# Kernel tuning notes

Hardware: AMD Instinct MI355X
Metric: run time of the kernel (lower is better)

Reference implementation:

```python
import jax, jax.numpy as jnp
import numpy as np

B, S, D, H, DH = 4, 2048, 1024, 16, 64  # batch, seq, d_model, heads, head_dim


def setup_inputs() -> dict:
    key = jax.random.key(0)
    ks = jax.random.split(key, 5)
    sc_in = 1.0 / np.sqrt(D)
    return {
        "x": jax.random.normal(ks[0], (B, S, D), dtype=jnp.float32),
        "Wq": jax.random.normal(ks[1], (H, D, DH), dtype=jnp.float32) * sc_in,
        "Wk": jax.random.normal(ks[2], (H, D, DH), dtype=jnp.float32) * sc_in,
        "Wv": jax.random.normal(ks[3], (H, D, DH), dtype=jnp.float32) * sc_in,
        "Wo": jax.random.normal(ks[4], (D, D), dtype=jnp.float32) * sc_in,
        "bo": jnp.zeros((D,), dtype=jnp.float32),
    }


def reference(x, Wq, Wk, Wv, Wo, bo):
    # Per-head Q/K/V projections (all heads batched in one einsum each).
    q = jnp.einsum("bsd,hde->bhse", x, Wq)  # [B,H,S,DH]
    k = jnp.einsum("bsd,hde->bhse", x, Wk)
    v = jnp.einsum("bsd,hde->bhse", x, Wv)
    scale = 1.0 / jnp.sqrt(jnp.asarray(DH, dtype=x.dtype))
    scores = jnp.einsum("bhse,bhte->bhst", q, k) * scale  # [B,H,S,S]
    causal = jnp.tril(jnp.ones((S, S), dtype=bool))
    scores = jnp.where(causal, scores, jnp.asarray(-jnp.inf, dtype=scores.dtype))
    attn = jax.nn.softmax(scores, axis=-1)
    heads = jnp.einsum("bhst,bhte->bhse", attn, v)  # [B,H,S,DH]
    # Concat heads (head-major order matches torch.cat of per-head outputs).
    concat = heads.transpose(0, 2, 1, 3).reshape(B, S, D)
    out = jnp.einsum("bsd,df->bsf", concat, Wo) + bo
    return out  # dropout_rate = 0.0 -> identity
```

## Files before the change

kernel.cpp:

```cpp
#include <hip/hip_runtime.h>
#include <hip/hip_bf16.h>

typedef __attribute__((ext_vector_type(8))) short short8;
typedef __attribute__((ext_vector_type(4))) short short4x;
typedef __attribute__((ext_vector_type(4))) float floatx4;

__device__ __forceinline__ short f2bf(float f) {
    unsigned u = __float_as_uint(f);
    u = u + 0x7fffu + ((u >> 16) & 1u);
    return (short)(u >> 16);
}
__device__ __forceinline__ short f2bf_rz(float f) {
    return (short)(__float_as_uint(f) >> 16);
}

static constexpr int B_ = 4, S_ = 2048, D_ = 1024, H_ = 16, DH_ = 64;
static constexpr float QSCALE = 0.125f * 1.4426950408889634f;

__global__ __launch_bounds__(256) void convert_x(const float* __restrict__ in,
                                                 short* __restrict__ out, int n8) {
    int i = blockIdx.x * 256 + threadIdx.x;
    if (i >= n8) return;
    const float4* p = (const float4*)(in + (size_t)i * 8);
    float4 a = p[0], b = p[1];
    short8 v;
    v[0] = f2bf(a.x); v[1] = f2bf(a.y); v[2] = f2bf(a.z); v[3] = f2bf(a.w);
    v[4] = f2bf(b.x); v[5] = f2bf(b.y); v[6] = f2bf(b.z); v[7] = f2bf(b.w);
    *(short8*)(out + (size_t)i * 8) = v;
}

__global__ __launch_bounds__(256) void prep_weights(const float* __restrict__ Wq,
                                                    const float* __restrict__ Wk,
                                                    const float* __restrict__ Wv,
                                                    const float* __restrict__ Wo,
                                                    short* __restrict__ WqT,
                                                    short* __restrict__ WkT,
                                                    short* __restrict__ WvT,
                                                    short* __restrict__ WoT) {
    __shared__ alignas(16) float t[64 * 68];
    int z = blockIdx.z;
    const float* in;
    short* out;
    int N, M = D_, n0;
    if (z < 3) {
        const float* I = (z == 0) ? Wq : (z == 1) ? Wk : Wv;
        short* O = (z == 0) ? WqT : (z == 1) ? WkT : WvT;
        in = I + (size_t)blockIdx.y * D_ * DH_;
        out = O + (size_t)blockIdx.y * D_ * DH_;
        N = DH_; n0 = 0;
    } else {
        in = Wo; out = WoT; N = D_; n0 = blockIdx.y * 64;
    }
    int m0 = blockIdx.x * 64;
    int tid = threadIdx.x;
#pragma unroll
    for (int i = 0; i < 4; ++i) {
        int c = tid + i * 256;
        int row = c >> 4, c4 = (c & 15) * 4;
        float4 v = *(const float4*)(in + (size_t)(m0 + row) * N + n0 + c4);
        *(float4*)(t + row * 68 + c4) = v;
    }
    __syncthreads();
#pragma unroll
    for (int i = 0; i < 2; ++i) {
        int c = tid + i * 256;
        int row = c >> 3, c8 = (c & 7) * 8;
        short8 v;
#pragma unroll
        for (int j = 0; j < 8; ++j) v[j] = f2bf(t[(c8 + j) * 68 + row]);
        *(short8*)(out + (size_t)(n0 + row) * M + m0 + c8) = v;
    }
}

__device__ __forceinline__ void gemm128_core(const short* __restrict__ A,
                                             const short* __restrict__ Bm,
                                             short* ldsA, short* ldsB,
                                             int m0, int n0,
                                             floatx4 (&acc)[4][4],
                                             int w, int lane, int quad, int lm) {
    const int K = 1024;
    int wm = (w >> 1) * 64, wn = (w & 1) * 64;
    int rsub = lane >> 3;
    int csw = ((lane & 7) ^ rsub) * 8;
    int lmx = lm & 7;
    for (int k0 = 0; k0 < K; k0 += 64) {
#pragma unroll
        for (int i = 0; i < 4; ++i) {
            int r0 = w * 32 + i * 8;
            const short* ga = A + (size_t)(m0 + r0 + rsub) * K + k0 + csw;
            __builtin_amdgcn_global_load_lds((const __attribute__((address_space(1))) void*)ga,
                                             (__attribute__((address_space(3))) void*)(ldsA + r0 * 64),
                                             16, 0, 0);
            const short* gb = Bm + (size_t)(n0 + r0 + rsub) * K + k0 + csw;
            __builtin_amdgcn_global_load_lds((const __attribute__((address_space(1))) void*)gb,
                                             (__attribute__((address_space(3))) void*)(ldsB + r0 * 64),
                                             16, 0, 0);
        }
        __syncthreads();
#pragma unroll
        for (int ks = 0; ks < 2; ++ks) {
            short8 am[4], bn[4];
#pragma unroll
            for (int i = 0; i < 4; ++i)
                am[i] = *(const short8*)(ldsA + (wm + i * 16 + lm) * 64 + (((ks * 4 + quad) ^ lmx) << 3));
#pragma unroll
            for (int i = 0; i < 4; ++i)
                bn[i] = *(const short8*)(ldsB + (wn + i * 16 + lm) * 64 + (((ks * 4 + quad) ^ lmx) << 3));
#pragma unroll
            for (int mi = 0; mi < 4; ++mi)
#pragma unroll
                for (int ni = 0; ni < 4; ++ni)
                    acc[mi][ni] = __builtin_amdgcn_mfma_f32_16x16x32_bf16(am[mi], bn[ni], acc[mi][ni], 0, 0, 0);
        }
        __syncthreads();
    }
}

__global__ __launch_bounds__(256, 3) void qkv_gemm128(const short* __restrict__ xb,
                                                      const short* __restrict__ WqT,
                                                      const short* __restrict__ WkT,
                                                      const short* __restrict__ WvT,
                                                      short* __restrict__ Q,
                                                      short* __restrict__ K,
                                                      short* __restrict__ VT) {
    __shared__ alignas(16) short lds[16384];
    short* ldsA = lds;
    short* ldsB = lds + 8192;
    int m0 = blockIdx.x * 128, n0 = blockIdx.y * 128, z = blockIdx.z;
    const short* Bm = (z == 0) ? WqT : (z == 1) ? WkT : WvT;
    int tid = threadIdx.x, w = tid >> 6, lane = tid & 63, quad = lane >> 4, lm = lane & 15;

    floatx4 acc[4][4];
#pragma unroll
    for (int mi = 0; mi < 4; ++mi)
#pragma unroll
        for (int ni = 0; ni < 4; ++ni) acc[mi][ni] = (floatx4)0.0f;

    gemm128_core(xb, Bm, ldsA, ldsB, m0, n0, acc, w, lane, quad, lm);

    int wm = (w >> 1) * 64, wn = (w & 1) * 64;
    int b = m0 >> 11;
    int sbase = m0 & 2047;

    if (z < 2) {
        short* O = (z == 0) ? Q : K;
        float scale = (z == 0) ? QSCALE : 1.0f;
        short* t = lds;
#pragma unroll
        for (int ph = 0; ph < 2; ++ph) {
            if (ph) __syncthreads();
            if ((w & 1) == ph) {
#pragma unroll
                for (int mi = 0; mi < 4; ++mi)
#pragma unroll
                    for (int ni = 0; ni < 4; ++ni)
#pragma unroll
                        for (int r = 0; r < 4; ++r)
                            t[(wm + mi * 16 + quad * 4 + r) * 68 + ni * 16 + lm] =
                                f2bf(acc[mi][ni][r] * scale);
            }
            __syncthreads();
            int h = (n0 + ph * 64) >> 6;
            size_t obase = ((size_t)(b * 16 + h) * 2048 + sbase) * 64;
#pragma unroll
            for (int i = 0; i < 4; ++i) {
                int c = tid + i * 256;
                int m = c >> 3, e8 = (c & 7) * 8;
                short8 v = *(const short8*)(t + m * 68 + e8);
                *(short8*)(O + obase + (size_t)m * 64 + e8) = v;
            }
        }
    } else {
        short* t = lds;
#pragma unroll
        for (int ph = 0; ph < 2; ++ph) {
            if (ph) __syncthreads();
            if ((w & 1) == ph) {
#pragma unroll
                for (int mi = 0; mi < 4; ++mi)
#pragma unroll
                    for (int ni = 0; ni < 4; ++ni) {
                        int nl = ni * 16 + lm;
#pragma unroll
                        for (int r = 0; r < 4; ++r) {
                            int ml = wm + mi * 16 + quad * 4 + r;
                            t[nl * 136 + ml] = f2bf(acc[mi][ni][r]);
                        }
                    }
            }
            __syncthreads();
#pragma unroll
            for (int i = 0; i < 4; ++i) {
                int c = tid + i * 256;
                int rowl = c >> 4, colc = (c & 15) * 8;
                short8 v = *(const short8*)(t + rowl * 136 + colc);
                size_t n = n0 + ph * 64 + rowl;
                *(short8*)(VT + ((size_t)b * 1024 + n) * 2048 + sbase + colc) = v;
            }
        }
    }
}

__global__ __launch_bounds__(256, 3) void outproj128(const short* __restrict__ CC,
                                                     const short* __restrict__ WoT,
                                                     const float* __restrict__ bo,
                                                     float* __restrict__ out) {
    __shared__ alignas(16) short lds[16384];
    short* ldsA = lds;
    short* ldsB = lds + 8192;
    int m0 = blockIdx.x * 128, n0 = blockIdx.y * 128;
    int tid = threadIdx.x, w = tid >> 6, lane = tid & 63, quad = lane >> 4, lm = lane & 15;

    floatx4 acc[4][4];
#pragma unroll
    for (int mi = 0; mi < 4; ++mi)
#pragma unroll
        for (int ni = 0; ni < 4; ++ni) acc[mi][ni] = (floatx4)0.0f;

    gemm128_core(CC, WoT, ldsA, ldsB, m0, n0, acc, w, lane, quad, lm);

    int wm = (w >> 1) * 64, wn = (w & 1) * 64;
#pragma unroll
    for (int mi = 0; mi < 4; ++mi)
#pragma unroll
        for (int ni = 0; ni < 4; ++ni) {
            int n = n0 + wn + ni * 16 + lm;
            float bb = bo[n];
#pragma unroll
            for (int r = 0; r < 4; ++r) {
                int m = m0 + wm + mi * 16 + quad * 4 + r;
                out[(size_t)m * 1024 + n] = acc[mi][ni][r] + bb;
            }
        }
}

__global__ __launch_bounds__(256, 2) void attn_kernel(const short* __restrict__ Q,
                                                      const short* __restrict__ Kb,
                                                      const short* __restrict__ VT,
                                                      short* __restrict__ CC) {
    __shared__ alignas(16) short Kt[128 * 64];
    __shared__ alignas(16) short Vt[64 * 128];
    __shared__ alignas(16) short Pt[128 * 128];
    int bh = blockIdx.x;
    int pi = blockIdx.y;
    int b = bh >> 4, h = bh & 15;
    int tid = threadIdx.x;
    int w = tid >> 6, l = tid & 63;
    int quad = l >> 4, lm = l & 15;
    int lmx = lm & 7;
    int rsub = l >> 3;
    int csw = ((l & 7) ^ rsub) * 8;
    int vr4 = l >> 4;
    int vc = l & 15;

    const short* Qbh = Q + (size_t)bh * S_ * DH_;
    const short* Kbh = Kb + (size_t)bh * S_ * DH_;
    const short* Vbh = VT + (size_t)bh * 64 * S_;

    for (int ps = 0; ps < 2; ++ps) {
        int qt = ps ? (15 - pi) : pi;
        int q0 = qt * 128;

        short8 qa[2][2];
#pragma unroll
        for (int nq = 0; nq < 2; ++nq) {
            const short* Qrow = Qbh + (size_t)(q0 + nq * 64 + w * 16 + lm) * DH_;
            qa[nq][0] = *(const short8*)(Qrow + quad * 8);
            qa[nq][1] = *(const short8*)(Qrow + 32 + quad * 8);
        }

        floatx4 acc_o[2][4];
#pragma unroll
        for (int nq = 0; nq < 2; ++nq)
#pragma unroll
            for (int ct = 0; ct < 4; ++ct) acc_o[nq][ct] = (floatx4)0.0f;
        float lsum[2] = {0.0f, 0.0f};

        int nkt = qt + 1;
        for (int kt = 0; kt < nkt; ++kt) {
            int t0 = kt * 128;
            const short* Ktile = Kbh + (size_t)t0 * DH_;
#pragma unroll
            for (int i = 0; i < 4; ++i) {
                int r0 = w * 32 + i * 8;
                const short* ga = Ktile + (size_t)(r0 + rsub) * 64 + csw;
                __builtin_amdgcn_global_load_lds((const __attribute__((address_space(1))) void*)ga,
                                                 (__attribute__((address_space(3))) void*)(Kt + r0 * 64),
                                                 16, 0, 0);
            }
#pragma unroll
            for (int i = 0; i < 4; ++i) {
                int r0v = w * 16 + i * 4;
                int row = r0v + vr4;
                const short* gv = Vbh + (size_t)row * S_ + t0 + ((vc ^ (row & 7)) * 8);
                __builtin_amdgcn_global_load_lds((const __attribute__((address_space(1))) void*)gv,
                                                 (__attribute__((address_space(3))) void*)(Vt + r0v * 128),
                                                 16, 0, 0);
            }
            __syncthreads();

            short8 kf[8][2];
#pragma unroll
            for (int mt = 0; mt < 8; ++mt)
#pragma unroll
                for (int ks = 0; ks < 2; ++ks)
                    kf[mt][ks] = *(const short8*)(Kt + (mt * 16 + lm) * 64 + (((ks * 4 + quad) ^ lmx) << 3));

            bool last = (kt == nkt - 1);
#pragma unroll
            for (int nq = 0; nq < 2; ++nq) {
                floatx4 sc[8];
                __builtin_amdgcn_s_setprio(1);
#pragma unroll
                for (int mt = 0; mt < 8; ++mt) {
                    floatx4 t = (floatx4)0.0f;
                    t = __builtin_amdgcn_mfma_f32_16x16x32_bf16(kf[mt][0], qa[nq][0], t, 0, 0, 0);
                    t = __builtin_amdgcn_mfma_f32_16x16x32_bf16(kf[mt][1], qa[nq][1], t, 0, 0, 0);
                    sc[mt] = t;
                }
                __builtin_amdgcn_s_setprio(0);
                if (last) {
                    int q_ = q0 + nq * 64 + w * 16 + lm;
#pragma unroll
                    for (int mt = 0; mt < 8; ++mt)
#pragma unroll
                        for (int r = 0; r < 4; ++r) {
                            int t_ = t0 + mt * 16 + quad * 4 + r;
                            if (t_ > q_) sc[mt][r] = -INFINITY;
                        }
                }
                int prow = nq * 64 + w * 16 + lm;
#pragma unroll
                for (int mt = 0; mt < 8; ++mt) {
                    float p0 = exp2f(sc[mt][0]);
                    float p1 = exp2f(sc[mt][1]);
                    float p2 = exp2f(sc[mt][2]);
                    float p3 = exp2f(sc[mt][3]);
                    lsum[nq] += (p0 + p1) + (p2 + p3);
                    short4x pk;
                    pk[0] = f2bf_rz(p0); pk[1] = f2bf_rz(p1);
                    pk[2] = f2bf_rz(p2); pk[3] = f2bf_rz(p3);
                    int c = mt * 2 + (quad >> 1);
                    *(short4x*)(Pt + prow * 128 + ((c ^ lmx) << 3) + (quad & 1) * 4) = pk;
                }
            }
            short8 pa[2][4];
#pragma unroll
            for (int nq = 0; nq < 2; ++nq)
#pragma unroll
                for (int ks = 0; ks < 4; ++ks)
                    pa[nq][ks] = *(const short8*)(Pt + (nq * 64 + w * 16 + lm) * 128 +
                                                  (((ks * 4 + quad) ^ lmx) << 3));
            __builtin_amdgcn_s_setprio(1);
#pragma unroll
            for (int ct = 0; ct < 4; ++ct) {
                const short* vrow = Vt + (ct * 16 + lm) * 128;
#pragma unroll
                for (int ks = 0; ks < 4; ++ks) {
                    short8 v = *(const short8*)(vrow + (((ks * 4 + quad) ^ lmx) << 3));
                    acc_o[0][ct] = __builtin_amdgcn_mfma_f32_16x16x32_bf16(pa[0][ks], v, acc_o[0][ct], 0, 0, 0);
                    acc_o[1][ct] = __builtin_amdgcn_mfma_f32_16x16x32_bf16(pa[1][ks], v, acc_o[1][ct], 0, 0, 0);
                }
            }
            __builtin_amdgcn_s_setprio(0);
            __syncthreads();
        }

        float invl[2];
#pragma unroll
        for (int nq = 0; nq < 2; ++nq) {
            float lr = lsum[nq];
            lr += __shfl_xor(lr, 16);
            lr += __shfl_xor(lr, 32);
            invl[nq] = 1.0f / lr;
        }

#pragma unroll
        for (int nq = 0; nq < 2; ++nq) {
#pragma unroll
            for (int r = 0; r < 4; ++r) {
                float iv = __shfl(invl[nq], quad * 4 + r);
                int row = q0 + nq * 64 + w * 16 + quad * 4 + r;
                short* OC = CC + ((size_t)b * S_ + row) * D_ + h * DH_;
#pragma unroll
                for (int ct = 0; ct < 4; ++ct)
                    OC[ct * 16 + lm] = f2bf(acc_o[nq][ct][r] * iv);
            }
        }
    }
}

extern "C" void kernel_launch(void* const* d_in, const int* in_sizes, int n_in,
                              void* d_out, int out_size, void* d_ws, size_t ws_size,
                              hipStream_t stream) {
    const float* x  = (const float*)d_in[0];
    const float* Wq = (const float*)d_in[1];
    const float* Wk = (const float*)d_in[2];
    const float* Wv = (const float*)d_in[3];
    const float* Wo = (const float*)d_in[4];
    const float* bo = (const float*)d_in[5];
    float* out = (float*)d_out;
    short* ws = (short*)d_ws;

    const size_t WSZ = (size_t)H_ * D_ * DH_;
    const size_t QSZ = (size_t)B_ * H_ * S_ * DH_;
    short* WqT = ws;
    short* WkT = WqT + WSZ;
    short* WvT = WkT + WSZ;
    short* WoT = WvT + WSZ;
    short* xb  = WoT + (size_t)D_ * D_;
    short* Qb  = xb + (size_t)B_ * S_ * D_;
    short* Kb  = Qb + QSZ;
    short* VTb = Kb + QSZ;
    short* CCb = VTb + QSZ;

    convert_x<<<(B_ * S_ * D_ / 8 + 255) / 256, 256, 0, stream>>>(x, xb, B_ * S_ * D_ / 8);
    prep_weights<<<dim3(16, 16, 4), 256, 0, stream>>>(Wq, Wk, Wv, Wo, WqT, WkT, WvT, WoT);
    qkv_gemm128<<<dim3(64, 8, 3), 256, 0, stream>>>(xb, WqT, WkT, WvT, Qb, Kb, VTb);
    attn_kernel<<<dim3(64, 8), 256, 0, stream>>>(Qb, Kb, VTb, CCb);
    outproj128<<<dim3(64, 8), 256, 0, stream>>>(CCb, WoT, bo, out);
}
```

Measured before the change: 243.0 us.

## Switch attention to 32x32x16 MFMA and keep P in registers via permlane swap

Rewrites the attention inner loop to use 32x32x16 bf16 MFMAs, computing S^T tiles whose accumulator layout can be converted to the PV operand layout in registers with v_cvt_pk_bf16_f32 and v_permlane32_swap. This removes the P shared-memory buffer and its write/read round trip plus the block's LDS footprint, and fewer larger MFMAs cut instruction count. P rounding changes from truncation to round-to-nearest. The cost is larger accumulator register use and reliance on gfx950-specific instructions.

```diff
diff --git a/kernel.cpp b/kernel.cpp
--- a/kernel.cpp
+++ b/kernel.cpp
@@ -4,6 +4,8 @@
 typedef __attribute__((ext_vector_type(8))) short short8;
 typedef __attribute__((ext_vector_type(4))) short short4x;
 typedef __attribute__((ext_vector_type(4))) float floatx4;
+typedef __attribute__((ext_vector_type(16))) float floatx16;
+typedef __attribute__((ext_vector_type(4))) unsigned uintx4;
 
 __device__ __forceinline__ short f2bf(float f) {
     unsigned u = __float_as_uint(f);
@@ -240,14 +242,12 @@
                                                       short* __restrict__ CC) {
     __shared__ alignas(16) short Kt[128 * 64];
     __shared__ alignas(16) short Vt[64 * 128];
-    __shared__ alignas(16) short Pt[128 * 128];
     int bh = blockIdx.x;
     int pi = blockIdx.y;
     int b = bh >> 4, h = bh & 15;
     int tid = threadIdx.x;
     int w = tid >> 6, l = tid & 63;
-    int quad = l >> 4, lm = l & 15;
-    int lmx = lm & 7;
+    int hi = l >> 5, l31 = l & 31, l7 = l & 7;
     int rsub = l >> 3;
     int csw = ((l & 7) ^ rsub) * 8;
     int vr4 = l >> 4;
@@ -260,21 +260,18 @@
     for (int ps = 0; ps < 2; ++ps) {
         int qt = ps ? (15 - pi) : pi;
         int q0 = qt * 128;
-
-        short8 qa[2][2];
-#pragma unroll
-        for (int nq = 0; nq < 2; ++nq) {
-            const short* Qrow = Qbh + (size_t)(q0 + nq * 64 + w * 16 + lm) * DH_;
-            qa[nq][0] = *(const short8*)(Qrow + quad * 8);
-            qa[nq][1] = *(const short8*)(Qrow + 32 + quad * 8);
-        }
-
-        floatx4 acc_o[2][4];
-#pragma unroll
-        for (int nq = 0; nq < 2; ++nq)
-#pragma unroll
-            for (int ct = 0; ct < 4; ++ct) acc_o[nq][ct] = (floatx4)0.0f;
-        float lsum[2] = {0.0f, 0.0f};
+        int qrow = q0 + w * 32 + l31;
+
+        short8 qa[4];
+        const short* Qrow = Qbh + (size_t)qrow * DH_;
+#pragma unroll
+        for (int ks = 0; ks < 4; ++ks)
+            qa[ks] = *(const short8*)(Qrow + ks * 16 + hi * 8);
+
+        floatx16 acc[2];
+        acc[0] = (floatx16)0.0f;
+        acc[1] = (floatx16)0.0f;
+        float lsum = 0.0f;
 
         int nkt = qt + 1;
         for (int kt = 0; kt < nkt; ++kt) {
@@ -299,93 +296,87 @@
             }
             __syncthreads();
 
-            short8 kf[8][2];
-#pragma unroll
-            for (int mt = 0; mt < 8; ++mt)
-#pragma unroll
-                for (int ks = 0; ks < 2; ++ks)
-                    kf[mt][ks] = *(const short8*)(Kt + (mt * 16 + lm) * 64 + (((ks * 4 + quad) ^ lmx) << 3));
-
-            bool last = (kt == nkt - 1);
-#pragma unroll
-            for (int nq = 0; nq < 2; ++nq) {
-                floatx4 sc[8];
-                __builtin_amdgcn_s_setprio(1);
-#pragma unroll
-                for (int mt = 0; mt < 8; ++mt) {
-                    floatx4 t = (floatx4)0.0f;
-                    t = __builtin_amdgcn_mfma_f32_16x16x32_bf16(kf[mt][0], qa[nq][0], t, 0, 0, 0);
-                    t = __builtin_amdgcn_mfma_f32_16x16x32_bf16(kf[mt][1], qa[nq][1], t, 0, 0, 0);
-                    sc[mt] = t;
+            floatx16 st[4];
+            __builtin_amdgcn_s_setprio(1);
+#pragma unroll
+            for (int tb = 0; tb < 4; ++tb) {
+                floatx16 t = (floatx16)0.0f;
+#pragma unroll
+                for (int ks = 0; ks < 4; ++ks) {
+                    short8 kf = *(const short8*)(Kt + (tb * 32 + l31) * 64 +
+                                                 (((ks * 2 + hi) ^ l7) << 3));
+                    t = __builtin_amdgcn_mfma_f32_32x32x16_bf16(kf, qa[ks], t, 0, 0, 0);
                 }
-                __builtin_amdgcn_s_setprio(0);
-                if (last) {
-                    int q_ = q0 + nq * 64 + w * 16 + lm;
-#pragma unroll
-                    for (int mt = 0; mt < 8; ++mt)
-#pragma unroll
-                        for (int r = 0; r < 4; ++r) {
-                            int t_ = t0 + mt * 16 + quad * 4 + r;
-                            if (t_ > q_) sc[mt][r] = -INFINITY;
-                        }
+                st[tb] = t;
+            }
+            __builtin_amdgcn_s_setprio(0);
+
+            if (kt == nkt - 1) {
+#pragma unroll
+                for (int tb = 0; tb < 4; ++tb)
+#pragma unroll
+                    for (int r = 0; r < 16; ++r) {
+                        int t_ = t0 + tb * 32 + (r & 3) + 8 * (r >> 2) + 4 * hi;
+                        if (t_ > qrow) st[tb][r] = -INFINITY;
+                    }
+            }
+
+#pragma unroll
+            for (int tb = 0; tb < 4; ++tb)
+#pragma unroll
+                for (int r = 0; r < 16; r += 4) {
+                    float p0 = exp2f(st[tb][r]);
+                    float p1 = exp2f(st[tb][r + 1]);
+                    float p2 = exp2f(st[tb][r + 2]);
+                    float p3 = exp2f(st[tb][r + 3]);
+                    st[tb][r] = p0; st[tb][r + 1] = p1;
+                    st[tb][r + 2] = p2; st[tb][r + 3] = p3;
+                    lsum += (p0 + p1) + (p2 + p3);
                 }
-                int prow = nq * 64 + w * 16 + lm;
-#pragma unroll
-                for (int mt = 0; mt < 8; ++mt) {
-                    float p0 = exp2f(sc[mt][0]);
-                    float p1 = exp2f(sc[mt][1]);
-                    float p2 = exp2f(sc[mt][2]);
-                    float p3 = exp2f(sc[mt][3]);
-                    lsum[nq] += (p0 + p1) + (p2 + p3);
-                    short4x pk;
-                    pk[0] = f2bf_rz(p0); pk[1] = f2bf_rz(p1);
-                    pk[2] = f2bf_rz(p2); pk[3] = f2bf_rz(p3);
-                    int c = mt * 2 + (quad >> 1);
-                    *(short4x*)(Pt + prow * 128 + ((c ^ lmx) << 3) + (quad & 1) * 4) = pk;
+
+            __builtin_amdgcn_s_setprio(1);
+#pragma unroll
+            for (int tb = 0; tb < 4; ++tb)
+#pragma unroll
+                for (int sl = 0; sl < 2; ++sl) {
+                    unsigned x0, y0, x1, y1;
+                    asm("v_cvt_pk_bf16_f32 %0, %1, %2" : "=v"(x0)
+                        : "v"(st[tb][sl * 8 + 0]), "v"(st[tb][sl * 8 + 1]));
+                    asm("v_cvt_pk_bf16_f32 %0, %1, %2" : "=v"(y0)
+                        : "v"(st[tb][sl * 8 + 4]), "v"(st[tb][sl * 8 + 5]));
+                    asm("v_cvt_pk_bf16_f32 %0, %1, %2" : "=v"(x1)
+                        : "v"(st[tb][sl * 8 + 2]), "v"(st[tb][sl * 8 + 3]));
+                    asm("v_cvt_pk_bf16_f32 %0, %1, %2" : "=v"(y1)
+                        : "v"(st[tb][sl * 8 + 6]), "v"(st[tb][sl * 8 + 7]));
+                    asm("v_permlane32_swap_b32 %0, %1" : "+v"(x0), "+v"(y0));
+                    asm("v_permlane32_swap_b32 %0, %1" : "+v"(x1), "+v"(y1));
+                    uintx4 pd;
+                    pd[0] = x0; pd[1] = x1; pd[2] = y0; pd[3] = y1;
+                    short8 pa = __builtin_bit_cast(short8, pd);
+                    int s = tb * 2 + sl;
+#pragma unroll
+                    for (int eb = 0; eb < 2; ++eb) {
+                        short8 v = *(const short8*)(Vt + (eb * 32 + l31) * 128 +
+                                                    (((s * 2 + hi) ^ l7) << 3));
+                        acc[eb] = __builtin_amdgcn_mfma_f32_32x32x16_bf16(pa, v, acc[eb], 0, 0, 0);
+                    }
                 }
-            }
-            short8 pa[2][4];
-#pragma unroll
-            for (int nq = 0; nq < 2; ++nq)
-#pragma unroll
-                for (int ks = 0; ks < 4; ++ks)
-                    pa[nq][ks] = *(const short8*)(Pt + (nq * 64 + w * 16 + lm) * 128 +
-                                                  (((ks * 4 + quad) ^ lmx) << 3));
-            __builtin_amdgcn_s_setprio(1);
-#pragma unroll
-            for (int ct = 0; ct < 4; ++ct) {
-                const short* vrow = Vt + (ct * 16 + lm) * 128;
-#pragma unroll
-                for (int ks = 0; ks < 4; ++ks) {
-                    short8 v = *(const short8*)(vrow + (((ks * 4 + quad) ^ lmx) << 3));
-                    acc_o[0][ct] = __builtin_amdgcn_mfma_f32_16x16x32_bf16(pa[0][ks], v, acc_o[0][ct], 0, 0, 0);
-                    acc_o[1][ct] = __builtin_amdgcn_mfma_f32_16x16x32_bf16(pa[1][ks], v, acc_o[1][ct], 0, 0, 0);
-                }
-            }
             __builtin_amdgcn_s_setprio(0);
             __syncthreads();
         }
 
-        float invl[2];
-#pragma unroll
-        for (int nq = 0; nq < 2; ++nq) {
-            float lr = lsum[nq];
-            lr += __shfl_xor(lr, 16);
-            lr += __shfl_xor(lr, 32);
-            invl[nq] = 1.0f / lr;
-        }
-
-#pragma unroll
-        for (int nq = 0; nq < 2; ++nq) {
-#pragma unroll
-            for (int r = 0; r < 4; ++r) {
-                float iv = __shfl(invl[nq], quad * 4 + r);
-                int row = q0 + nq * 64 + w * 16 + quad * 4 + r;
-                short* OC = CC + ((size_t)b * S_ + row) * D_ + h * DH_;
-#pragma unroll
-                for (int ct = 0; ct < 4; ++ct)
-                    OC[ct * 16 + lm] = f2bf(acc_o[nq][ct][r] * iv);
-            }
+        float lt = lsum + __shfl_xor(lsum, 32);
+        float invl = 1.0f / lt;
+
+#pragma unroll
+        for (int r = 0; r < 16; ++r) {
+            int q_local = (r & 3) + 8 * (r >> 2) + 4 * hi;
+            float iv = __shfl(invl, q_local);
+            int row = q0 + w * 32 + q_local;
+            short* OC = CC + ((size_t)b * S_ + row) * D_ + h * DH_;
+#pragma unroll
+            for (int eb = 0; eb < 2; ++eb)
+                OC[eb * 32 + l31] = f2bf(acc[eb][r] * iv);
         }
     }
 }
```

Result: faster. 235.6 us (median of 2 runs) (-3.1%).
